# Optimization experiments

Hardware: AMD Instinct MI355X
Metric: run time of the kernel (lower is better)

## Reference

```python
import jax, jax.numpy as jnp
import numpy as np

RATIO = 0.2
MIX_ALPHA = 0.5
TEMPERATURE = 0.1
EPS = 1e-12  # F.normalize eps


def setup_inputs() -> dict:
    key = jax.random.key(0)
    z = jax.random.normal(key, (16384, 256), dtype=jnp.float32)
    return {"z": z}


def reference(z):
    B = z.shape[0]
    n_hard = max(1, int(B * RATIO))

    # L2-normalize rows (F.normalize with eps clamp)
    norm = jnp.maximum(jnp.linalg.norm(z, axis=-1, keepdims=True), EPS)
    z_norm = z / norm

    # [B, B] cosine similarity, diagonal excluded
    sim = z_norm @ z_norm.T
    diag = jnp.eye(B, dtype=bool)
    sim = jnp.where(diag, -jnp.inf, sim)
    logits = sim / TEMPERATURE  # softmax(logits) == sim_probs

    # Batched sampling: replaces the per-sample Python loop with one fused pass
    key = jax.random.key(42)
    k_src, k_tgt, k_alpha = jax.random.split(key, 3)
    src_idx = jax.random.randint(k_src, (n_hard,), 0, B)  # torch.randint
    # categorical over logits rows == multinomial over softmax probs
    tgt_idx = jax.random.categorical(k_tgt, logits[src_idx], axis=-1)
    alpha = jax.random.uniform(k_alpha, (n_hard, 1), dtype=z.dtype) * MIX_ALPHA

    hard_negs = alpha * z[src_idx] + (1.0 - alpha) * z[tgt_idx]  # [n_hard, D]
    return hard_negs
```

## Files before the change

kernel.cpp:

```cpp
#include <hip/hip_runtime.h>
#include <stdint.h>
#include <math.h>

#define BN 16384
#define DK 256
#define NH 3276
#define NJB 52
#define NCB 128
#define NTILE (NJB * NCB)

typedef __attribute__((ext_vector_type(8))) short short8;
typedef __attribute__((ext_vector_type(4))) short short4v;
typedef __attribute__((ext_vector_type(4))) float f32x4;

__host__ __device__ __forceinline__ void tf2x32(uint32_t k0, uint32_t k1,
                                                uint32_t c0, uint32_t c1,
                                                uint32_t& o0, uint32_t& o1) {
  uint32_t ks2 = 0x1BD11BDAu ^ k0 ^ k1;
  uint32_t x0 = c0 + k0, x1 = c1 + k1;
#define RR(d) { x0 += x1; x1 = __builtin_rotateleft32(x1, d); x1 ^= x0; }
  RR(13) RR(15) RR(26) RR(6)   x0 += k1;  x1 += ks2 + 1u;
  RR(17) RR(29) RR(16) RR(24)  x0 += ks2; x1 += k0  + 2u;
  RR(13) RR(15) RR(26) RR(6)   x0 += k0;  x1 += k1  + 3u;
  RR(17) RR(29) RR(16) RR(24)  x0 += k1;  x1 += ks2 + 4u;
  RR(13) RR(15) RR(26) RR(6)   x0 += ks2; x1 += k0  + 5u;
#undef RR
  o0 = x0; o1 = x1;
}

__device__ __forceinline__ uint32_t rand32_at(uint32_t k0, uint32_t k1, uint32_t p) {
  uint32_t x0, x1; tf2x32(k0, k1, 0u, p, x0, x1);
  return x0 ^ x1;
}

__device__ __forceinline__ float unif01_from_bits(uint32_t bits) {
  return __uint_as_float((bits >> 9) | 0x3f800000u) - 1.0f;
}

__device__ __forceinline__ float gumbel_at(uint32_t k0, uint32_t k1, uint32_t p) {
  uint32_t bits = rand32_at(k0, k1, p);
  float f = unif01_from_bits(bits);
  float u = fmaxf(f, 1.17549435e-38f);
  float t = __log2f(u) * (-0.69314718055994531f);
  return __log2f(t) * (-0.69314718055994531f);
}

__device__ __forceinline__ unsigned long long packvc(float v, uint32_t c) {
  uint32_t u = __float_as_uint(v);
  u ^= ((int32_t)u < 0) ? 0xFFFFFFFFu : 0x80000000u;
  return ((unsigned long long)u << 32) | (unsigned long long)(~c);
}

__device__ __forceinline__ void glds16(const unsigned short* g, short* l) {
  __builtin_amdgcn_global_load_lds(
      (const __attribute__((address_space(1))) void*)g,
      (__attribute__((address_space(3))) void*)l, 16, 0, 0);
}

__global__ __launch_bounds__(256) void k_prep(const float* __restrict__ z,
                                              unsigned short* __restrict__ zh,
                                              unsigned short* __restrict__ zl,
                                              int* __restrict__ src_idx,
                                              unsigned long long* __restrict__ best,
                                              uint32_t k20, uint32_t k21) {
  int b = blockIdx.x, t = threadIdx.x;
  if (b < BN / 4) {
    int row = b * 4 + (t >> 6), lane = t & 63;
    float4 v = *(const float4*)&z[row * DK + lane * 4];
    float ss = v.x * v.x + v.y * v.y + v.z * v.z + v.w * v.w;
#pragma unroll
    for (int off = 32; off; off >>= 1) ss += __shfl_xor(ss, off, 64);
    float inv = 1.0f / fmaxf(sqrtf(ss), 1e-12f);
    float f[4] = {v.x * inv, v.y * inv, v.z * inv, v.w * inv};
    short4v h, l;
#pragma unroll
    for (int i = 0; i < 4; ++i) {
      uint32_t u = __float_as_uint(f[i]);
      h[i] = (short)(u >> 16);
      float r = f[i] - __uint_as_float(u & 0xFFFF0000u);
      l[i] = (short)(__float_as_uint(r) >> 16);
    }
    *(short4v*)&zh[row * DK + lane * 4] = h;
    *(short4v*)&zl[row * DK + lane * 4] = l;
  } else {
    int i = (b - BN / 4) * 256 + t;
    if (i < NH) {
      uint32_t bits = rand32_at(k20, k21, (uint32_t)i);
      src_idx[i] = (int)(bits & (uint32_t)(BN - 1));
      best[i] = 0ull;
    }
  }
}

__global__ __launch_bounds__(256, 5) void k_main(const unsigned short* __restrict__ zh,
                                                 const unsigned short* __restrict__ zl,
                                                 const int* __restrict__ src_idx,
                                                 unsigned long long* __restrict__ best,
                                                 uint32_t kt0, uint32_t kt1) {
  __shared__ __align__(16) short As_hi[64 * 32];
  __shared__ __align__(16) short As_lo[64 * 32];
  __shared__ __align__(16) short Bs_hi[128 * 32];
  __shared__ __align__(16) short Bs_lo[128 * 32];

  const int flat = blockIdx.x;
  const int xcd = flat & 7, slot = flat >> 3;
  const int c_base = (xcd * 16 + (slot & 15)) * 128;
  const int j_base = (slot >> 4) * 64;

  const int t = threadIdx.x;
  const int lane = t & 63, w = t >> 6;

  const int ra = w * 16 + (lane >> 2);
  const int rb0 = w * 32 + (lane >> 2);
  const int rb1 = rb0 + 16;
  const int ua = (lane & 3) ^ ((ra >> 1) & 3);
  const int ub0 = (lane & 3) ^ ((rb0 >> 1) & 3);
  const int ub1 = (lane & 3) ^ ((rb1 >> 1) & 3);
  const uint32_t offA = (uint32_t)(src_idx[min(j_base + ra, NH - 1)] * DK + ua * 8);
  const uint32_t offB0 = (uint32_t)((c_base + rb0) * DK + ub0 * 8);
  const uint32_t offB1 = (uint32_t)((c_base + rb1) * DK + ub1 * 8);
  short* dA  = &As_hi[w * 512];
  short* dAl = &As_lo[w * 512];
  short* dB  = &Bs_hi[w * 1024];
  short* dBl = &Bs_lo[w * 1024];

  const int mh = w >> 1, ch = w & 1;
  const int cl = lane & 15, q = lane >> 4;
  int foffA[2], foffB[4];
#pragma unroll
  for (int i = 0; i < 2; ++i) {
    int r = mh * 32 + cl + i * 16;
    foffA[i] = r * 32 + (q ^ ((r >> 1) & 3)) * 8;
  }
#pragma unroll
  for (int i = 0; i < 4; ++i) {
    int r = ch * 64 + cl + i * 16;
    foffB[i] = r * 32 + (q ^ ((r >> 1) & 3)) * 8;
  }

  const int q4 = q * 4;
  const int coff = c_base + ch * 64;
  const int roff = j_base + mh * 32;
  const uint32_t ccl = (uint32_t)(coff + cl);

  f32x4 acc[2][4];
#pragma unroll
  for (int mt = 0; mt < 2; ++mt)
#pragma unroll
    for (int nt = 0; nt < 4; ++nt) acc[mt][nt] = (f32x4){0.f, 0.f, 0.f, 0.f};

  glds16(zh + offA, dA);
  glds16(zl + offA, dAl);
  glds16(zh + offB0, dB);
  glds16(zh + offB1, dB + 512);
  glds16(zl + offB0, dBl);
  glds16(zl + offB1, dBl + 512);

#pragma unroll
  for (int kc = 0; kc < 8; ++kc) {
    __syncthreads();

    short8 ah[2], al[2], bh[4], bl[4];
#pragma unroll
    for (int nt = 0; nt < 4; ++nt) {
      bh[nt] = *(const short8*)&Bs_hi[foffB[nt]];
      bl[nt] = *(const short8*)&Bs_lo[foffB[nt]];
    }
#pragma unroll
    for (int mt = 0; mt < 2; ++mt) {
      ah[mt] = *(const short8*)&As_hi[foffA[mt]];
      al[mt] = *(const short8*)&As_lo[foffA[mt]];
    }
    __syncthreads();

    if (kc < 7) {
      const int ko = (kc + 1) * 32;
      glds16(zh + offA + ko, dA);
      glds16(zl + offA + ko, dAl);
      glds16(zh + offB0 + ko, dB);
      glds16(zh + offB1 + ko, dB + 512);
      glds16(zl + offB0 + ko, dBl);
      glds16(zl + offB1 + ko, dBl + 512);
    }

#pragma unroll
    for (int mt = 0; mt < 2; ++mt)
#pragma unroll
      for (int nt = 0; nt < 4; ++nt) {
        acc[mt][nt] = __builtin_amdgcn_mfma_f32_16x16x32_bf16(ah[mt], bh[nt], acc[mt][nt], 0, 0, 0);
        acc[mt][nt] = __builtin_amdgcn_mfma_f32_16x16x32_bf16(ah[mt], bl[nt], acc[mt][nt], 0, 0, 0);
        acc[mt][nt] = __builtin_amdgcn_mfma_f32_16x16x32_bf16(al[mt], bh[nt], acc[mt][nt], 0, 0, 0);
      }
  }

  const uint32_t pbase = (uint32_t)(roff + q4) * (uint32_t)BN + ccl;
#pragma unroll
  for (int mt = 0; mt < 2; ++mt)
#pragma unroll
    for (int r = 0; r < 4; ++r) {
      int gj = roff + mt * 16 + q4 + r;
      int s = src_idx[min(gj, NH - 1)];
      float bv = -INFINITY; uint32_t bc = 0;
#pragma unroll
      for (int nt = 0; nt < 4; ++nt) {
        uint32_t c = ccl + (uint32_t)(nt * 16);
        uint32_t p = pbase + (uint32_t)((mt * 16 + r) * BN + nt * 16);
        float gv = gumbel_at(kt0, kt1, p);
        float tot = fmaf(acc[mt][nt][r], 10.0f, gv);
        tot = ((int)c == s) ? -INFINITY : tot;
        if (tot > bv) { bv = tot; bc = c; }
      }
      unsigned long long key = packvc(bv, bc);
#pragma unroll
      for (int off = 1; off <= 8; off <<= 1) {
        unsigned long long o = __shfl_xor(key, off, 64);
        if (o > key) key = o;
      }
      if (cl == 0 && gj < NH) atomicMax(&best[gj], key);
    }
}

__global__ __launch_bounds__(64) void k_out(const float* __restrict__ z,
                                            const int* __restrict__ src_idx,
                                            const unsigned long long* __restrict__ best,
                                            float* __restrict__ out,
                                            uint32_t ka0, uint32_t ka1) {
  int j = blockIdx.x;
  int lane = threadIdx.x;
  int s = src_idx[j];
  int tgt = (int)(~((uint32_t)(best[j] & 0xFFFFFFFFull)));
  uint32_t bits = rand32_at(ka0, ka1, (uint32_t)j);
  float alpha = unif01_from_bits(bits) * 0.5f;
  float om = 1.0f - alpha;
  float4 a = *(const float4*)&z[s * DK + lane * 4];
  float4 b = *(const float4*)&z[tgt * DK + lane * 4];
  float4 o;
  o.x = alpha * a.x + om * b.x;
  o.y = alpha * a.y + om * b.y;
  o.z = alpha * a.z + om * b.z;
  o.w = alpha * a.w + om * b.w;
  *(float4*)&out[j * DK + lane * 4] = o;
}

extern "C" void kernel_launch(void* const* d_in, const int* in_sizes, int n_in,
                              void* d_out, int out_size, void* d_ws, size_t ws_size,
                              hipStream_t stream) {
  const float* z = (const float*)d_in[0];
  float* out = (float*)d_out;
  char* ws = (char*)d_ws;
  int*                src_idx = (int*)(ws);
  unsigned long long* best    = (unsigned long long*)(ws + 16384);
  unsigned short*     zh      = (unsigned short*)(ws + 65536);
  unsigned short*     zl      = (unsigned short*)(ws + 65536 + 8388608);

  uint32_t r0 = 0u, r1 = 42u;
  uint32_t ks0, ks1, kt0, kt1, ka0, ka1, k20, k21;
  tf2x32(r0, r1, 0u, 0u, ks0, ks1);
  tf2x32(r0, r1, 0u, 1u, kt0, kt1);
  tf2x32(r0, r1, 0u, 2u, ka0, ka1);
  tf2x32(ks0, ks1, 0u, 1u, k20, k21);

  k_prep<<<dim3(BN / 4 + (NH + 255) / 256), dim3(256), 0, stream>>>(
      z, zh, zl, src_idx, best, k20, k21);
  k_main<<<dim3(NTILE), dim3(256), 0, stream>>>(zh, zl, src_idx, best, kt0, kt1);
  k_out <<<dim3(NH), dim3(64), 0, stream>>>(z, src_idx, best, out, ka0, ka1);
}
```

Baseline: 251.1 us.

## Shrink column tile to 64 and interleave Gumbel RNG with MFMA k-loop

Halves the column tile per block (64x64 instead of 64x128), doubling the block count and raising the occupancy hint to 6. The Gumbel noise for each output element is now computed inside the k-loop, two values per iteration, and kept in registers. The aim is to overlap the ALU-heavy Threefry hashing with MFMA work and global-to-LDS loads rather than running it serially in the epilogue. In exchange, the A tile is reloaded twice as often per column, more atomicMax calls are issued, and 16 extra registers are live through the loop.

```diff
diff --git a/kernel.cpp b/kernel.cpp
--- a/kernel.cpp
+++ b/kernel.cpp
@@ -6,7 +6,7 @@
 #define DK 256
 #define NH 3276
 #define NJB 52
-#define NCB 128
+#define NCB 256
 #define NTILE (NJB * NCB)
 
 typedef __attribute__((ext_vector_type(8))) short short8;
@@ -92,84 +92,72 @@
   }
 }
 
-__global__ __launch_bounds__(256, 5) void k_main(const unsigned short* __restrict__ zh,
+__global__ __launch_bounds__(256, 6) void k_main(const unsigned short* __restrict__ zh,
                                                  const unsigned short* __restrict__ zl,
                                                  const int* __restrict__ src_idx,
                                                  unsigned long long* __restrict__ best,
                                                  uint32_t kt0, uint32_t kt1) {
   __shared__ __align__(16) short As_hi[64 * 32];
   __shared__ __align__(16) short As_lo[64 * 32];
-  __shared__ __align__(16) short Bs_hi[128 * 32];
-  __shared__ __align__(16) short Bs_lo[128 * 32];
+  __shared__ __align__(16) short Bs_hi[64 * 32];
+  __shared__ __align__(16) short Bs_lo[64 * 32];
 
   const int flat = blockIdx.x;
   const int xcd = flat & 7, slot = flat >> 3;
-  const int c_base = (xcd * 16 + (slot & 15)) * 128;
-  const int j_base = (slot >> 4) * 64;
+  const int c_base = (xcd * 32 + (slot & 31)) * 64;
+  const int j_base = (slot >> 5) * 64;
 
   const int t = threadIdx.x;
   const int lane = t & 63, w = t >> 6;
 
-  const int ra = w * 16 + (lane >> 2);
-  const int rb0 = w * 32 + (lane >> 2);
-  const int rb1 = rb0 + 16;
-  const int ua = (lane & 3) ^ ((ra >> 1) & 3);
-  const int ub0 = (lane & 3) ^ ((rb0 >> 1) & 3);
-  const int ub1 = (lane & 3) ^ ((rb1 >> 1) & 3);
-  const uint32_t offA = (uint32_t)(src_idx[min(j_base + ra, NH - 1)] * DK + ua * 8);
-  const uint32_t offB0 = (uint32_t)((c_base + rb0) * DK + ub0 * 8);
-  const uint32_t offB1 = (uint32_t)((c_base + rb1) * DK + ub1 * 8);
+  const int rs = t >> 2;
+  const int u = (t & 3) ^ ((rs >> 1) & 3);
+  const uint32_t offA = (uint32_t)(src_idx[min(j_base + rs, NH - 1)] * DK + u * 8);
+  const uint32_t offB = (uint32_t)((c_base + rs) * DK + u * 8);
   short* dA  = &As_hi[w * 512];
   short* dAl = &As_lo[w * 512];
-  short* dB  = &Bs_hi[w * 1024];
-  short* dBl = &Bs_lo[w * 1024];
+  short* dB  = &Bs_hi[w * 512];
+  short* dBl = &Bs_lo[w * 512];
 
   const int mh = w >> 1, ch = w & 1;
   const int cl = lane & 15, q = lane >> 4;
-  int foffA[2], foffB[4];
+  int foffA[2], foffB[2];
 #pragma unroll
   for (int i = 0; i < 2; ++i) {
-    int r = mh * 32 + cl + i * 16;
-    foffA[i] = r * 32 + (q ^ ((r >> 1) & 3)) * 8;
+    int rA = mh * 32 + cl + i * 16;
+    foffA[i] = rA * 32 + (q ^ ((rA >> 1) & 3)) * 8;
+    int rB = ch * 32 + cl + i * 16;
+    foffB[i] = rB * 32 + (q ^ ((rB >> 1) & 3)) * 8;
   }
-#pragma unroll
-  for (int i = 0; i < 4; ++i) {
-    int r = ch * 64 + cl + i * 16;
-    foffB[i] = r * 32 + (q ^ ((r >> 1) & 3)) * 8;
-  }
 
   const int q4 = q * 4;
-  const int coff = c_base + ch * 64;
   const int roff = j_base + mh * 32;
-  const uint32_t ccl = (uint32_t)(coff + cl);
-
-  f32x4 acc[2][4];
+  const uint32_t ccl = (uint32_t)(c_base + ch * 32 + cl);
+
+  f32x4 acc[2][2];
 #pragma unroll
   for (int mt = 0; mt < 2; ++mt)
 #pragma unroll
-    for (int nt = 0; nt < 4; ++nt) acc[mt][nt] = (f32x4){0.f, 0.f, 0.f, 0.f};
+    for (int nt = 0; nt < 2; ++nt) acc[mt][nt] = (f32x4){0.f, 0.f, 0.f, 0.f};
+
+  float gum[16];
 
   glds16(zh + offA, dA);
   glds16(zl + offA, dAl);
-  glds16(zh + offB0, dB);
-  glds16(zh + offB1, dB + 512);
-  glds16(zl + offB0, dBl);
-  glds16(zl + offB1, dBl + 512);
+  glds16(zh + offB, dB);
+  glds16(zl + offB, dBl);
 
 #pragma unroll
   for (int kc = 0; kc < 8; ++kc) {
     __syncthreads();
 
-    short8 ah[2], al[2], bh[4], bl[4];
-#pragma unroll
-    for (int nt = 0; nt < 4; ++nt) {
-      bh[nt] = *(const short8*)&Bs_hi[foffB[nt]];
-      bl[nt] = *(const short8*)&Bs_lo[foffB[nt]];
-    }
-#pragma unroll
-    for (int mt = 0; mt < 2; ++mt) {
-      ah[mt] = *(const short8*)&As_hi[foffA[mt]];
-      al[mt] = *(const short8*)&As_lo[foffA[mt]];
+    short8 ah[2], al[2], bh[2], bl[2];
+#pragma unroll
+    for (int i = 0; i < 2; ++i) {
+      bh[i] = *(const short8*)&Bs_hi[foffB[i]];
+      bl[i] = *(const short8*)&Bs_lo[foffB[i]];
+      ah[i] = *(const short8*)&As_hi[foffA[i]];
+      al[i] = *(const short8*)&As_lo[foffA[i]];
     }
     __syncthreads();
 
@@ -177,23 +165,39 @@
       const int ko = (kc + 1) * 32;
       glds16(zh + offA + ko, dA);
       glds16(zl + offA + ko, dAl);
-      glds16(zh + offB0 + ko, dB);
-      glds16(zh + offB1 + ko, dB + 512);
-      glds16(zl + offB0 + ko, dBl);
-      glds16(zl + offB1 + ko, dBl + 512);
+      glds16(zh + offB + ko, dB);
+      glds16(zl + offB + ko, dBl);
     }
 
 #pragma unroll
     for (int mt = 0; mt < 2; ++mt)
 #pragma unroll
-      for (int nt = 0; nt < 4; ++nt) {
+      for (int nt = 0; nt < 2; ++nt) {
         acc[mt][nt] = __builtin_amdgcn_mfma_f32_16x16x32_bf16(ah[mt], bh[nt], acc[mt][nt], 0, 0, 0);
         acc[mt][nt] = __builtin_amdgcn_mfma_f32_16x16x32_bf16(ah[mt], bl[nt], acc[mt][nt], 0, 0, 0);
         acc[mt][nt] = __builtin_amdgcn_mfma_f32_16x16x32_bf16(al[mt], bh[nt], acc[mt][nt], 0, 0, 0);
       }
+
+    float gv0, gv1;
+    {
+      const int idx = kc * 2 + 0;
+      const int mt = idx >> 3, r = (idx >> 1) & 3, nt = idx & 1;
+      int gj = roff + mt * 16 + q4 + r;
+      uint32_t p = (uint32_t)gj * (uint32_t)BN + ccl + (uint32_t)(nt * 16);
+      gv0 = gumbel_at(kt0, kt1, p);
+    }
+    {
+      const int idx = kc * 2 + 1;
+      const int mt = idx >> 3, r = (idx >> 1) & 3, nt = idx & 1;
+      int gj = roff + mt * 16 + q4 + r;
+      uint32_t p = (uint32_t)gj * (uint32_t)BN + ccl + (uint32_t)(nt * 16);
+      gv1 = gumbel_at(kt0, kt1, p);
+    }
+    asm volatile("" : "+v"(gv0), "+v"(gv1));
+    gum[kc * 2 + 0] = gv0;
+    gum[kc * 2 + 1] = gv1;
   }
 
-  const uint32_t pbase = (uint32_t)(roff + q4) * (uint32_t)BN + ccl;
 #pragma unroll
   for (int mt = 0; mt < 2; ++mt)
 #pragma unroll
@@ -202,11 +206,9 @@
       int s = src_idx[min(gj, NH - 1)];
       float bv = -INFINITY; uint32_t bc = 0;
 #pragma unroll
-      for (int nt = 0; nt < 4; ++nt) {
+      for (int nt = 0; nt < 2; ++nt) {
         uint32_t c = ccl + (uint32_t)(nt * 16);
-        uint32_t p = pbase + (uint32_t)((mt * 16 + r) * BN + nt * 16);
-        float gv = gumbel_at(kt0, kt1, p);
-        float tot = fmaf(acc[mt][nt][r], 10.0f, gv);
+        float tot = fmaf(acc[mt][nt][r], 10.0f, gum[(mt * 4 + r) * 2 + nt]);
         tot = ((int)c == s) ? -INFINITY : tot;
         if (tot > bv) { bv = tot; bc = c; }
       }
```

New measurement: 309.7 us. +23.3%, slower.
